# Kernel optimization log

Measured on AMD Instinct MI355X. Metric: run time of the kernel, lower is better.

## Reference

```python
import jax, jax.numpy as jnp
import numpy as np

BETA = 0.25
EPS = 1e-10


def setup_inputs() -> dict:
    key = jax.random.key(0)
    k1, k2 = jax.random.split(key)
    B, D, K = 32768, 512, 8192
    a = jax.random.normal(k1, (B, D), dtype=jnp.float32)
    # torch init: uniform(-1/K, 1/K)
    codebook = jax.random.uniform(k2, (K, D), dtype=jnp.float32,
                                  minval=-1.0 / K, maxval=1.0 / K)
    return {"a": a, "codebook": codebook}


def reference(a, codebook):
    # a: [B, D], codebook: [K, D]
    B = a.shape[0]
    K = codebook.shape[0]
    # squared-distance via a2 + e2 - 2*a.E^T (no [B,K,D] intermediate)
    a2 = jnp.sum(a * a, axis=1, keepdims=True)            # [B, 1]
    e2 = jnp.sum(codebook * codebook, axis=1)[None, :]    # [1, K]
    dist = a2 + e2 - 2.0 * (a @ codebook.T)               # [B, K]
    idx = jnp.argmin(dist, axis=1)                        # [B] int
    z_q = codebook[idx]                                   # [B, D]
    # straight-through estimator
    z = a + jax.lax.stop_gradient(z_q - a)
    commit_loss = BETA * jnp.mean((a - jax.lax.stop_gradient(z_q)) ** 2)
    codebook_loss = jnp.mean((jax.lax.stop_gradient(a) - z_q) ** 2)
    # usage stats (no_grad in torch)
    usage = jnp.zeros((K,), a.dtype).at[idx].add(1.0) / B  # mean of one-hot
    perplexity = jnp.exp(-jnp.sum(usage * jnp.log(usage + EPS)))
    used_codes = jnp.sum(usage > 0).astype(a.dtype)
    usage_mean = jnp.mean(usage)
    return (idx, z, commit_loss, codebook_loss, perplexity, used_codes, usage_mean)
```

## Files before the change

### kernel.cpp

```cpp
#include <hip/hip_runtime.h>
#include <stdint.h>

#define D_DIM 512
#define ESTRIDE 528
#define SPLIT_K 384
#define DELTA 8.0e-4f
#define MAXC 48

typedef unsigned long long u64;
typedef float f32x4 __attribute__((ext_vector_type(4)));
typedef short s16x8 __attribute__((ext_vector_type(8)));

static __device__ inline unsigned short f2bf(float x) {
  unsigned u = __float_as_uint(x);
  u = (u + 0x7FFFu + ((u >> 16) & 1u)) >> 16;
  return (unsigned short)u;
}
static __device__ inline unsigned mono(float f) {
  unsigned u = __float_as_uint(f);
  return (u & 0x80000000u) ? ~u : (u | 0x80000000u);
}
static __device__ inline float unmono(unsigned m) {
  return __uint_as_float((m & 0x80000000u) ? (m & 0x7FFFFFFFu) : ~m);
}

__global__ void k_init(int* __restrict__ counts, int K) {
  int i = blockIdx.x * blockDim.x + threadIdx.x;
  if (i < K) counts[i] = 0;
}

__global__ void k_prep(const float* __restrict__ E, unsigned short* __restrict__ Ebf2,
                       float* __restrict__ Eskew, int* __restrict__ counts, int K) {
  int i = blockIdx.x * blockDim.x + threadIdx.x;
  if (i < K) counts[i] = 0;
  if (i >= K * 64) return;
  int row = i >> 6;
  int ch = i & 63;
  const float* src = E + (size_t)row * D_DIM + ch * 8;
  float4 f0 = *(const float4*)(src);
  float4 f1 = *(const float4*)(src + 4);
  s16x8 o;
  o[0] = (short)f2bf(f0.x); o[1] = (short)f2bf(f0.y);
  o[2] = (short)f2bf(f0.z); o[3] = (short)f2bf(f0.w);
  o[4] = (short)f2bf(f1.x); o[5] = (short)f2bf(f1.y);
  o[6] = (short)f2bf(f1.z); o[7] = (short)f2bf(f1.w);
  size_t slot = ((size_t)(row >> 7) * 16 + (size_t)(ch >> 2)) * 512 +
                (size_t)(row & 127) * 4 + (size_t)(ch & 3);
  *(s16x8*)(Ebf2 + slot * 8) = o;
  float* dst = Eskew + (size_t)row * ESTRIDE + ch * 8;
  *(float4*)(dst) = f0;
  *(float4*)(dst + 4) = f1;
}

__global__ void k_rowsq(const float* __restrict__ X, float* __restrict__ out, int nrows) {
  int t = threadIdx.x;
  int row = blockIdx.x * 4 + (t >> 6);
  int l = t & 63;
  if (row >= nrows) return;
  int b = l >> 4;
  int L = l & 15;
  const float* p = X + (size_t)row * D_DIM + b * 128 + L;
  float v[8];
#pragma unroll
  for (int j = 0; j < 8; ++j) {
    float x = p[16 * j];
    float sq = x * x;
    asm volatile("" : "+v"(sq));
    v[j] = sq;
  }
  float s = ((v[0] + v[1]) + (v[2] + v[3])) + ((v[4] + v[5]) + (v[6] + v[7]));
  s += __shfl_xor(s, 8, 64);
  s += __shfl_xor(s, 4, 64);
  s += __shfl_xor(s, 2, 64);
  s += __shfl_xor(s, 1, 64);
  s += __shfl_xor(s, 16, 64);
  s += __shfl_xor(s, 32, 64);
  if (l == 0) out[row] = s;
}

__global__ __launch_bounds__(512) void k_screen(
    const float* __restrict__ A, const unsigned short* __restrict__ Ebf2,
    const float* __restrict__ e2, int* __restrict__ cand_cnt,
    unsigned short* __restrict__ cand, int K) {
  __shared__ unsigned runmin[128];
  __shared__ unsigned cnt[128];
  __shared__ unsigned short list[128 * MAXC];
  __shared__ __align__(16) char Alds[128 * 1024];
  __shared__ __align__(16) char Blds[2 * 8192];

  const int t = threadIdx.x;
  const int m0 = blockIdx.x * 128;

  if (t < 128) { runmin[t] = 0xFFFFFFFFu; cnt[t] = 0; }

  {
    int row = t >> 2;
    int s4 = t & 3;
    const float* ar = A + (size_t)(m0 + row) * D_DIM;
#pragma unroll
    for (int c = 0; c < 16; ++c) {
      int ch = s4 * 16 + c;
      float4 f0 = *(const float4*)(ar + ch * 8);
      float4 f1 = *(const float4*)(ar + ch * 8 + 4);
      s16x8 o;
      o[0] = (short)f2bf(f0.x); o[1] = (short)f2bf(f0.y);
      o[2] = (short)f2bf(f0.z); o[3] = (short)f2bf(f0.w);
      o[4] = (short)f2bf(f1.x); o[5] = (short)f2bf(f1.y);
      o[6] = (short)f2bf(f1.z); o[7] = (short)f2bf(f1.w);
      int off = ((row * 64 + ch) * 16) ^ ((row & 15) << 4);
      *(s16x8*)(Alds + off) = o;
    }
  }

  const int lane = t & 63;
  const int wid = t >> 6;
  const int wm = wid >> 2;
  const int wn = wid & 3;
  const int l15 = lane & 15;
  const int lhi = lane >> 4;

#define ISSUE_CHUNK(C)                                                          \
  {                                                                             \
    const unsigned short* _src = Ebf2 + ((size_t)(C) * 512 + t) * 8;            \
    __builtin_amdgcn_global_load_lds(                                           \
        (const __attribute__((address_space(1))) unsigned int*)_src,            \
        (__attribute__((address_space(3))) unsigned int*)(Blds + ((C) & 1) * 8192 + wid * 1024), \
        16, 0, 0);                                                              \
  }

  ISSUE_CHUNK(0)
  __syncthreads();

  for (int tile = 0; tile < 64; ++tile) {
    const int n0 = tile * 128;

    f32x4 acc[4][2];
#pragma unroll
    for (int r = 0; r < 4; ++r)
#pragma unroll
      for (int c = 0; c < 2; ++c) acc[r][c] = (f32x4){0.f, 0.f, 0.f, 0.f};

#pragma unroll
    for (int kk = 0; kk < 16; ++kk) {
      const int c = tile * 16 + kk;
      if (c + 1 < 1024) ISSUE_CHUNK(c + 1)

      const char* Bc = Blds + (c & 1) * 8192;
      s16x8 b0 = *(const s16x8*)(Bc + ((wn * 32 + l15) * 4 + lhi) * 16);
      s16x8 b1 = *(const s16x8*)(Bc + ((wn * 32 + 16 + l15) * 4 + lhi) * 16);
      s16x8 af[4];
#pragma unroll
      for (int r = 0; r < 4; ++r) {
        int row = wm * 64 + r * 16 + l15;
        int off = ((row * 64 + kk * 4 + lhi) * 16) ^ ((row & 15) << 4);
        af[r] = *(const s16x8*)(Alds + off);
      }
#pragma unroll
      for (int r = 0; r < 4; ++r) {
        acc[r][0] = __builtin_amdgcn_mfma_f32_16x16x32_bf16(af[r], b0, acc[r][0], 0, 0, 0);
        acc[r][1] = __builtin_amdgcn_mfma_f32_16x16x32_bf16(af[r], b1, acc[r][1], 0, 0, 0);
      }
      __syncthreads();
    }

    float e2c0 = e2[n0 + wn * 32 + l15];
    float e2c1 = e2[n0 + wn * 32 + 16 + l15];
#pragma unroll
    for (int r = 0; r < 4; ++r)
#pragma unroll
      for (int g = 0; g < 4; ++g) {
        float s0 = fmaf(-2.f, acc[r][0][g], e2c0);
        float s1 = fmaf(-2.f, acc[r][1][g], e2c1);
        int row = wm * 64 + r * 16 + lhi * 4 + g;
        float mn = fminf(s0, s1);
        mn = fminf(mn, __shfl_xor(mn, 1, 64));
        mn = fminf(mn, __shfl_xor(mn, 2, 64));
        mn = fminf(mn, __shfl_xor(mn, 4, 64));
        mn = fminf(mn, __shfl_xor(mn, 8, 64));
        if (l15 == 0) atomicMin(&runmin[row], mono(mn));
        float thr = unmono(runmin[row]) + DELTA;
        if (s0 <= thr) {
          unsigned p = atomicAdd(&cnt[row], 1u);
          if (p < MAXC) list[row * MAXC + p] = (unsigned short)(n0 + wn * 32 + l15);
        }
        if (s1 <= thr) {
          unsigned p = atomicAdd(&cnt[row], 1u);
          if (p < MAXC) list[row * MAXC + p] = (unsigned short)(n0 + wn * 32 + 16 + l15);
        }
      }
  }
  __syncthreads();
  {
    int row = t >> 2;
    unsigned c = cnt[row];
    if ((t & 3) == 0) cand_cnt[m0 + row] = (int)c;
    unsigned cc = c < MAXC ? c : MAXC;
    for (unsigned p = t & 3; p < cc; p += 4)
      cand[(size_t)(m0 + row) * MAXC + p] = list[row * MAXC + p];
  }
}

static __device__ inline u64 exact_pack(const float* __restrict__ ar,
                                        const float* __restrict__ er,
                                        float a2r, float e2k, int k) {
  float acc1 = 0.f, acc2 = 0.f;
  for (int d = 0; d < SPLIT_K; d += 4) {
    float4 a = *(const float4*)(ar + d);
    float4 e = *(const float4*)(er + d);
    acc1 = fmaf(a.x, e.x, acc1); acc1 = fmaf(a.y, e.y, acc1);
    acc1 = fmaf(a.z, e.z, acc1); acc1 = fmaf(a.w, e.w, acc1);
  }
  for (int d = SPLIT_K; d < D_DIM; d += 4) {
    float4 a = *(const float4*)(ar + d);
    float4 e = *(const float4*)(er + d);
    acc2 = fmaf(a.x, e.x, acc2); acc2 = fmaf(a.y, e.y, acc2);
    acc2 = fmaf(a.z, e.z, acc2); acc2 = fmaf(a.w, e.w, acc2);
  }
  float M = acc1 + acc2;
  float S = a2r + e2k;
  float s = fmaf(-2.f, M, S);
  return ((u64)mono(s) << 32) | (unsigned)k;
}

__global__ __launch_bounds__(256) void k_rescore(
    const float* __restrict__ A, const float* __restrict__ Eskew,
    const float* __restrict__ a2, const float* __restrict__ e2,
    const int* __restrict__ cand_cnt, const unsigned short* __restrict__ cand,
    float* __restrict__ out_idx, float* __restrict__ out_z,
    float* __restrict__ rowsum, int* __restrict__ counts, int K) {
  int lane = threadIdx.x & 63;
  int r = blockIdx.x * 4 + (threadIdx.x >> 6);
  int c = cand_cnt[r];
  const float* ar = A + (size_t)r * D_DIM;
  float a2r = a2[r];
  u64 best = ~0ULL;
  if (c <= MAXC) {
    if (lane < c) {
      int k = cand[(size_t)r * MAXC + lane];
      best = exact_pack(ar, Eskew + (size_t)k * ESTRIDE, a2r, e2[k], k);
    }
  } else {
    for (int k = lane; k < K; k += 64) {
      u64 p = exact_pack(ar, Eskew + (size_t)k * ESTRIDE, a2r, e2[k], k);
      if (p < best) best = p;
    }
  }
#pragma unroll
  for (int m = 1; m < 64; m <<= 1) {
    u64 o = __shfl_xor(best, m, 64);
    if (o < best) best = o;
  }
  int idx = (int)(unsigned)(best & 0xFFFFFFFFULL);

  const float4* pa = (const float4*)(ar) + lane * 2;
  const float4* pe = (const float4*)(Eskew + (size_t)idx * ESTRIDE) + lane * 2;
  float4* pz = (float4*)(out_z + (size_t)r * D_DIM) + lane * 2;
  float ls = 0.f;
#pragma unroll
  for (int q = 0; q < 2; ++q) {
    float4 a = pa[q];
    float4 e = pe[q];
    float4 z;
    z.x = a.x + (e.x - a.x);
    z.y = a.y + (e.y - a.y);
    z.z = a.z + (e.z - a.z);
    z.w = a.w + (e.w - a.w);
    pz[q] = z;
    float dx = a.x - e.x, dy = a.y - e.y, dz = a.z - e.z, dw = a.w - e.w;
    ls += dx * dx + dy * dy + dz * dz + dw * dw;
  }
#pragma unroll
  for (int m = 1; m < 64; m <<= 1) ls += __shfl_xor(ls, m, 64);
  if (lane == 0) {
    out_idx[r] = (float)idx;
    rowsum[r] = ls;
    atomicAdd(&counts[idx], 1);
  }
}

#define KTILE(D0, ACC)                                                          \
  {                                                                             \
    int r = t >> 2;                                                             \
    int c4 = (t & 3) << 2;                                                      \
    float4 va = *(const float4*)(A + (size_t)(m0 + r) * D_DIM + (D0) + c4);     \
    As[c4 + 0][r] = va.x; As[c4 + 1][r] = va.y;                                 \
    As[c4 + 2][r] = va.z; As[c4 + 3][r] = va.w;                                 \
    float4 vb = *(const float4*)(E + (size_t)(n0 + r) * D_DIM + (D0) + c4);     \
    Es[c4 + 0][r] = vb.x; Es[c4 + 1][r] = vb.y;                                 \
    Es[c4 + 2][r] = vb.z; Es[c4 + 3][r] = vb.w;                                 \
    __syncthreads();                                                            \
    _Pragma("unroll")                                                           \
    for (int dd = 0; dd < 16; ++dd) {                                           \
      float af[4], bf[8];                                                       \
      *(float4*)af = *(const float4*)(&As[dd][ty * 4]);                         \
      *(float4*)bf = *(const float4*)(&Es[dd][tx * 4]);                         \
      *(float4*)(bf + 4) = *(const float4*)(&Es[dd][64 + tx * 4]);              \
      _Pragma("unroll")                                                         \
      for (int i = 0; i < 4; ++i)                                               \
        _Pragma("unroll")                                                       \
        for (int j = 0; j < 8; ++j)                                             \
          ACC[i][j] = fmaf(af[i], bf[j], ACC[i][j]);                            \
    }                                                                           \
    __syncthreads();                                                            \
  }

__global__ __launch_bounds__(512) void k_argmin_f32(
    const float* __restrict__ A, const float* __restrict__ E,
    const float* __restrict__ a2, const float* __restrict__ e2,
    float* __restrict__ out_idx, int* __restrict__ idx_ws, int K) {
  __shared__ float As[16][128];
  __shared__ float Es[16][128];
  const int m0 = blockIdx.x * 128;
  const int t = threadIdx.x;
  const int tx = t & 15;
  const int ty = t >> 4;
  float a2l[4];
#pragma unroll
  for (int i = 0; i < 4; ++i) a2l[i] = a2[m0 + ty * 4 + i];
  u64 best[4];
#pragma unroll
  for (int i = 0; i < 4; ++i) best[i] = ~0ULL;
  for (int n0 = 0; n0 < K; n0 += 128) {
    float acc1[4][8], acc2[4][8];
#pragma unroll
    for (int i = 0; i < 4; ++i)
#pragma unroll
      for (int j = 0; j < 8; ++j) { acc1[i][j] = 0.f; acc2[i][j] = 0.f; }
    for (int d0 = 0; d0 < SPLIT_K; d0 += 16) KTILE(d0, acc1)
    for (int d0 = SPLIT_K; d0 < D_DIM; d0 += 16) KTILE(d0, acc2)
    float e2l[8];
#pragma unroll
    for (int j = 0; j < 8; ++j) {
      int cl = (j < 4) ? (tx * 4 + j) : (64 + tx * 4 + (j - 4));
      e2l[j] = e2[n0 + cl];
    }
#pragma unroll
    for (int i = 0; i < 4; ++i) {
#pragma unroll
      for (int j = 0; j < 8; ++j) {
        int cl = (j < 4) ? (tx * 4 + j) : (64 + tx * 4 + (j - 4));
        float S = a2l[i] + e2l[j];
        float m = acc1[i][j] + acc2[i][j];
        float s = fmaf(-2.f, m, S);
        u64 p = ((u64)mono(s) << 32) | (unsigned)(n0 + cl);
        if (p < best[i]) best[i] = p;
      }
    }
  }
#pragma unroll
  for (int m = 1; m < 16; m <<= 1) {
#pragma unroll
    for (int i = 0; i < 4; ++i) {
      u64 o = __shfl_xor(best[i], m, 64);
      if (o < best[i]) best[i] = o;
    }
  }
  if (tx == 0) {
#pragma unroll
    for (int i = 0; i < 4; ++i) {
      int row = m0 + ty * 4 + i;
      int idx = (int)(unsigned)(best[i] & 0xFFFFFFFFULL);
      out_idx[row] = (float)idx;
      idx_ws[row] = idx;
    }
  }
}

__global__ void k_gather(const float* __restrict__ A, const float* __restrict__ E,
                         const int* __restrict__ idx_ws,
                         float* __restrict__ out_z, float* __restrict__ rowsum,
                         int* __restrict__ counts) {
  int b = blockIdx.x;
  int t = threadIdx.x;
  int idx = idx_ws[b];
  const float4* pa = (const float4*)(A + (size_t)b * D_DIM);
  const float4* pe = (const float4*)(E + (size_t)idx * D_DIM);
  float4 a = pa[t];
  float4 e = pe[t];
  float4 z;
  z.x = a.x + (e.x - a.x);
  z.y = a.y + (e.y - a.y);
  z.z = a.z + (e.z - a.z);
  z.w = a.w + (e.w - a.w);
  ((float4*)(out_z + (size_t)b * D_DIM))[t] = z;
  float dx = a.x - e.x, dy = a.y - e.y, dz = a.z - e.z, dw = a.w - e.w;
  float ls = dx * dx + dy * dy + dz * dz + dw * dw;
#pragma unroll
  for (int off = 32; off > 0; off >>= 1) ls += __shfl_down(ls, off, 64);
  __shared__ float wsum[2];
  if ((t & 63) == 0) wsum[t >> 6] = ls;
  __syncthreads();
  if (t == 0) {
    rowsum[b] = wsum[0] + wsum[1];
    atomicAdd(&counts[idx], 1);
  }
}

__global__ void k_stats(const int* __restrict__ counts, const float* __restrict__ rowsum,
                        float* __restrict__ out_sc, int B, int K) {
  int t = threadIdx.x;
  double ent = 0.0, tot = 0.0, S = 0.0;
  int used = 0;
  for (int k = t; k < K; k += 256) {
    int c = counts[k];
    double u = (double)c / (double)B;
    ent += u * log(u + 1e-10);
    tot += u;
    used += (c > 0) ? 1 : 0;
  }
  for (int b = t; b < B; b += 256) S += (double)rowsum[b];
  __shared__ double se[256];
  __shared__ double st[256];
  __shared__ double ss[256];
  __shared__ int su[256];
  se[t] = ent; st[t] = tot; ss[t] = S; su[t] = used;
  __syncthreads();
  for (int s = 128; s > 0; s >>= 1) {
    if (t < s) { se[t] += se[t + s]; st[t] += st[t + s]; ss[t] += ss[t + s]; su[t] += su[t + s]; }
    __syncthreads();
  }
  if (t == 0) {
    double Sm = ss[0];
    double N = (double)B * (double)D_DIM;
    out_sc[0] = (float)(0.25 * Sm / N);
    out_sc[1] = (float)(Sm / N);
    out_sc[2] = (float)exp(-se[0]);
    out_sc[3] = (float)su[0];
    out_sc[4] = (float)(st[0] / (double)K);
  }
}

extern "C" void kernel_launch(void* const* d_in, const int* in_sizes, int n_in,
                              void* d_out, int out_size, void* d_ws, size_t ws_size,
                              hipStream_t stream) {
  const float* A = (const float*)d_in[0];
  const float* E = (const float*)d_in[1];
  const int B = in_sizes[0] / D_DIM;
  const int K = in_sizes[1] / D_DIM;

  float* out = (float*)d_out;
  float* out_idx = out;
  float* out_z = out + B;
  float* out_sc = out + B + (size_t)B * D_DIM;

  char* ws = (char*)d_ws;
  size_t off = 0;
  float* a2 = (float*)(ws + off); off += (size_t)B * 4;
  float* e2 = (float*)(ws + off); off += (size_t)K * 4;
  int* counts = (int*)(ws + off); off += (size_t)K * 4;
  float* rowsum = (float*)(ws + off); off += (size_t)B * 4;
  int* idx_ws = (int*)(ws + off); off += (size_t)B * 4;
  int* cand_cnt = (int*)(ws + off); off += (size_t)B * 4;
  unsigned short* cand = (unsigned short*)(ws + off); off += (size_t)B * MAXC * 2;
  unsigned short* Ebf2 = (unsigned short*)(ws + off); off += (size_t)K * 512 * 2;
  float* Eskew = (float*)(ws + off); off += (size_t)K * ESTRIDE * 4;
  const size_t need = off;

  k_rowsq<<<(B + 3) / 4, 256, 0, stream>>>(A, a2, B);
  k_rowsq<<<(K + 3) / 4, 256, 0, stream>>>(E, e2, K);

  if (ws_size >= need) {
    int np = K * 64;
    k_prep<<<(np + 255) / 256, 256, 0, stream>>>(E, Ebf2, Eskew, counts, K);
    k_screen<<<B / 128, 512, 0, stream>>>(A, Ebf2, e2, cand_cnt, cand, K);
    k_rescore<<<B / 4, 256, 0, stream>>>(A, Eskew, a2, e2, cand_cnt, cand,
                                         out_idx, out_z, rowsum, counts, K);
  } else {
    k_init<<<(K + 255) / 256, 256, 0, stream>>>(counts, K);
    k_argmin_f32<<<B / 128, 512, 0, stream>>>(A, E, a2, e2, out_idx, idx_ws, K);
    k_gather<<<B, 128, 0, stream>>>(A, E, idx_ws, out_z, rowsum, counts);
  }
  k_stats<<<1, 256, 0, stream>>>(counts, rowsum, out_sc, B, K);
}
```

Measured before the change: 1.078 ms.

## Triple-buffer codebook chunks with one barrier per step and direct candidate writes

```diff
diff --git a/kernel.cpp b/kernel.cpp
--- a/kernel.cpp
+++ b/kernel.cpp
@@ -45,7 +45,7 @@
   o[4] = (short)f2bf(f1.x); o[5] = (short)f2bf(f1.y);
   o[6] = (short)f2bf(f1.z); o[7] = (short)f2bf(f1.w);
   size_t slot = ((size_t)(row >> 7) * 16 + (size_t)(ch >> 2)) * 512 +
-                (size_t)(row & 127) * 4 + (size_t)(ch & 3);
+                (size_t)(ch & 3) * 128 + (size_t)(row & 127);
   *(s16x8*)(Ebf2 + slot * 8) = o;
   float* dst = Eskew + (size_t)row * ESTRIDE + ch * 8;
   *(float4*)(dst) = f0;
@@ -84,14 +84,32 @@
     unsigned short* __restrict__ cand, int K) {
   __shared__ unsigned runmin[128];
   __shared__ unsigned cnt[128];
-  __shared__ unsigned short list[128 * MAXC];
   __shared__ __align__(16) char Alds[128 * 1024];
-  __shared__ __align__(16) char Blds[2 * 8192];
+  __shared__ __align__(16) char Blds[3 * 8192];
 
   const int t = threadIdx.x;
   const int m0 = blockIdx.x * 128;
 
   if (t < 128) { runmin[t] = 0xFFFFFFFFu; cnt[t] = 0; }
+
+  const int lane = t & 63;
+  const int wid = t >> 6;
+  const int wm = wid >> 2;
+  const int wn = wid & 3;
+  const int l15 = lane & 15;
+  const int lhi = lane >> 4;
+
+#define ISSUE_CHUNK(C, BI)                                                      \
+  {                                                                             \
+    const unsigned short* _src = Ebf2 + ((size_t)(C) * 512 + t) * 8;            \
+    __builtin_amdgcn_global_load_lds(                                           \
+        (const __attribute__((address_space(1))) unsigned int*)_src,            \
+        (__attribute__((address_space(3))) unsigned int*)(Blds + (BI) * 8192 + wid * 1024), \
+        16, 0, 0);                                                              \
+  }
+
+  ISSUE_CHUNK(0, 0)
+  ISSUE_CHUNK(1, 1)
 
   {
     int row = t >> 2;
@@ -111,26 +129,9 @@
       *(s16x8*)(Alds + off) = o;
     }
   }
-
-  const int lane = t & 63;
-  const int wid = t >> 6;
-  const int wm = wid >> 2;
-  const int wn = wid & 3;
-  const int l15 = lane & 15;
-  const int lhi = lane >> 4;
-
-#define ISSUE_CHUNK(C)                                                          \
-  {                                                                             \
-    const unsigned short* _src = Ebf2 + ((size_t)(C) * 512 + t) * 8;            \
-    __builtin_amdgcn_global_load_lds(                                           \
-        (const __attribute__((address_space(1))) unsigned int*)_src,            \
-        (__attribute__((address_space(3))) unsigned int*)(Blds + ((C) & 1) * 8192 + wid * 1024), \
-        16, 0, 0);                                                              \
-  }
-
-  ISSUE_CHUNK(0)
   __syncthreads();
 
+  int tb = 0;
   for (int tile = 0; tile < 64; ++tile) {
     const int n0 = tile * 128;
 
@@ -143,11 +144,17 @@
 #pragma unroll
     for (int kk = 0; kk < 16; ++kk) {
       const int c = tile * 16 + kk;
-      if (c + 1 < 1024) ISSUE_CHUNK(c + 1)
-
-      const char* Bc = Blds + (c & 1) * 8192;
-      s16x8 b0 = *(const s16x8*)(Bc + ((wn * 32 + l15) * 4 + lhi) * 16);
-      s16x8 b1 = *(const s16x8*)(Bc + ((wn * 32 + 16 + l15) * 4 + lhi) * 16);
+      if (c == 1023) { asm volatile("s_waitcnt vmcnt(0)" ::: "memory"); }
+      else          { asm volatile("s_waitcnt vmcnt(1)" ::: "memory"); }
+      __builtin_amdgcn_s_barrier();
+      int bs = tb + (kk % 3);      if (bs >= 3) bs -= 3;
+      if (c + 2 < 1024) {
+        int bi = tb + ((kk + 2) % 3); if (bi >= 3) bi -= 3;
+        ISSUE_CHUNK(c + 2, bi)
+      }
+      const char* Bc = Blds + bs * 8192;
+      s16x8 b0 = *(const s16x8*)(Bc + (lhi * 128 + wn * 32 + l15) * 16);
+      s16x8 b1 = *(const s16x8*)(Bc + (lhi * 128 + wn * 32 + 16 + l15) * 16);
       s16x8 af[4];
 #pragma unroll
       for (int r = 0; r < 4; ++r) {
@@ -160,8 +167,8 @@
         acc[r][0] = __builtin_amdgcn_mfma_f32_16x16x32_bf16(af[r], b0, acc[r][0], 0, 0, 0);
         acc[r][1] = __builtin_amdgcn_mfma_f32_16x16x32_bf16(af[r], b1, acc[r][1], 0, 0, 0);
       }
-      __syncthreads();
-    }
+    }
+    tb += 1; if (tb >= 3) tb -= 3;
 
     float e2c0 = e2[n0 + wn * 32 + l15];
     float e2c1 = e2[n0 + wn * 32 + 16 + l15];
@@ -181,23 +188,16 @@
         float thr = unmono(runmin[row]) + DELTA;
         if (s0 <= thr) {
           unsigned p = atomicAdd(&cnt[row], 1u);
-          if (p < MAXC) list[row * MAXC + p] = (unsigned short)(n0 + wn * 32 + l15);
+          if (p < MAXC) cand[(size_t)(m0 + row) * MAXC + p] = (unsigned short)(n0 + wn * 32 + l15);
         }
         if (s1 <= thr) {
           unsigned p = atomicAdd(&cnt[row], 1u);
-          if (p < MAXC) list[row * MAXC + p] = (unsigned short)(n0 + wn * 32 + 16 + l15);
+          if (p < MAXC) cand[(size_t)(m0 + row) * MAXC + p] = (unsigned short)(n0 + wn * 32 + 16 + l15);
         }
       }
   }
   __syncthreads();
-  {
-    int row = t >> 2;
-    unsigned c = cnt[row];
-    if ((t & 3) == 0) cand_cnt[m0 + row] = (int)c;
-    unsigned cc = c < MAXC ? c : MAXC;
-    for (unsigned p = t & 3; p < cc; p += 4)
-      cand[(size_t)(m0 + row) * MAXC + p] = list[row * MAXC + p];
-  }
+  if (t < 128) cand_cnt[m0 + t] = (int)cnt[t];
 }
 
 static __device__ inline u64 exact_pack(const float* __restrict__ ar,
```

Measured after the change: 1.078 ms. Within noise of the previous version (-0.0%).
